# Optimization experiments

Measured on AMD Instinct MI355X. Metric: run time of the kernel, lower is better.

## Reference

```python
import jax, jax.numpy as jnp
import numpy as np

FACTOR = 0.1   # init_kwargs factor
EPS = 1e-7
B, C, H, W = 256, 3, 224, 224


def setup_inputs() -> dict:
    key = jax.random.key(0)
    k1, k2, k3 = jax.random.split(key, 3)
    x = jax.random.normal(k1, (B, C, H, W), dtype=jnp.float32)
    shift_fy = jax.random.uniform(k2, (B,), dtype=jnp.float32)  # maps to torch.rand(1)
    shift_fx = jax.random.uniform(k3, (B,), dtype=jnp.float32)
    return {"x": x, "shift_fy": shift_fy, "shift_fx": shift_fx}


def _shift_axis(img, shift, axis, size):
    # Equivalent to torch in-place slice copy + zero-fill:
    #   shift>0: img[..., :size-shift] = img[..., shift:]; img[..., size-shift:] = 0
    #   shift<0: img[..., -shift:]   = img[..., :shift];  img[..., :-shift]   = 0
    # == roll by -shift, then zero positions j where j+shift is out of [0, size)
    idx = jnp.arange(size)
    rolled = jnp.roll(img, -shift, axis=axis)
    mask = (idx + shift >= 0) & (idx + shift < size)
    shp = [1, 1, 1]
    shp[axis] = size
    return rolled * mask.reshape(shp).astype(img.dtype)


def _per_image(img, fy, fx):
    # img: [C, H, W]
    h, w = img.shape[1], img.shape[2]
    # int(shift_factor * size) truncates toward zero -> jnp.trunc
    sy = jnp.trunc((fy * 2.0 - 1.0) * FACTOR * h).astype(jnp.int32)
    sx = jnp.trunc((fx * 2.0 - 1.0) * FACTOR * w).astype(jnp.int32)
    img = _shift_axis(img, sy, 1, h)
    img = _shift_axis(img, sx, 2, w)
    # standardize with unbiased std (torch.std default, ddof=1)
    n = img.size
    mean = jnp.mean(img)
    var = jnp.sum(jnp.square(img - mean)) / (n - 1)
    img = (img - mean) / (jnp.sqrt(var) + EPS)
    # min-max normalize
    mn = jnp.min(img)
    mx = jnp.max(img)
    return (img - mn) / (mx - mn)


def reference(x, shift_fy, shift_fx):
    # fully vectorized over the batch (original uses a Python per-image loop)
    return jax.vmap(_per_image)(x, shift_fy, shift_fx)
```

## Files before the change

kernel.cpp:

```cpp
#include <hip/hip_runtime.h>
#include <math.h>


constexpr int kC = 3, kH = 224, kW = 224;
constexpr int kCHW = kC * kH * kW;
constexpr int kROWS = kC * kH;
constexpr int kQPR  = kW / 4;
constexpr int kNQ   = kROWS * kQPR;
constexpr int TB    = 256;
constexpr int PARTS = 8;

__device__ __forceinline__ void shifts_for(const float* __restrict__ sfy,
                                           const float* __restrict__ sfx,
                                           int img, int& sy, int& sx)
{
    float ty = sfy[img] * 2.0f - 1.0f; ty *= 0.1f; ty *= (float)kH;
    sy = (int)truncf(ty);
    float tx = sfx[img] * 2.0f - 1.0f; tx *= 0.1f; tx *= (float)kW;
    sx = (int)truncf(tx);
}

__global__ __launch_bounds__(TB) void minmax_k(
    const float* __restrict__ x, const float* __restrict__ sfy,
    const float* __restrict__ sfx, float2* __restrict__ ws)
{
    const int img  = blockIdx.x / PARTS;
    const int part = blockIdx.x - img * PARTS;
    const float* __restrict__ xb = x + (size_t)img * kCHW;

    int sy, sx; shifts_for(sfy, sfx, img, sy, sx);

    const int rlo = sy > 0 ? sy : 0;
    const int rhi = kH + (sy < 0 ? sy : 0);
    const int clo = sx > 0 ? sx : 0;
    const int chi = kW + (sx < 0 ? sx : 0);

    float vmin = INFINITY, vmax = -INFINITY;

    for (int f = part * TB + threadIdx.x; f < kNQ; f += PARTS * TB) {
        const int rr = f / kQPR;
        const int q  = f - rr * kQPR;
        const int j  = rr % kH;
        const bool rok = (j >= rlo) & (j < rhi);
        const float4 v4 = *(const float4*)(xb + rr * kW + q * 4);
        const float* v = (const float*)&v4;
        #pragma unroll
        for (int k = 0; k < 4; ++k) {
            const int i = q * 4 + k;
            const float val = (rok & (i >= clo) & (i < chi)) ? v[k] : 0.0f;
            vmin = fminf(vmin, val);
            vmax = fmaxf(vmax, val);
        }
    }

    #pragma unroll
    for (int off = 32; off > 0; off >>= 1) {
        vmin = fminf(vmin, __shfl_down(vmin, off));
        vmax = fmaxf(vmax, __shfl_down(vmax, off));
    }
    __shared__ float smin[TB / 64], smax[TB / 64];
    const int wave = threadIdx.x >> 6, lane = threadIdx.x & 63;
    if (lane == 0) { smin[wave] = vmin; smax[wave] = vmax; }
    __syncthreads();
    if (threadIdx.x == 0) {
        float mn = smin[0], mx = smax[0];
        #pragma unroll
        for (int w2 = 1; w2 < TB / 64; ++w2) {
            mn = fminf(mn, smin[w2]);
            mx = fmaxf(mx, smax[w2]);
        }
        ws[img * PARTS + part] = make_float2(mn, mx);
    }
}

template <int R>
__device__ __forceinline__ void gather_norm(const float* __restrict__ xb,
                                            float* __restrict__ ob,
                                            int sy, int sx, float mn, float inv,
                                            int f0)
{
    for (int f = f0; f < kNQ; f += PARTS * TB) {
        const int rr = f / kQPR;
        const int q  = f - rr * kQPR;
        const int j  = rr % kH;
        const int c0 = rr - j;
        const int jj = j + sy;
        const bool rowok = (unsigned)jj < (unsigned)kH;
        const int jc = rowok ? jj : 0;
        const float* __restrict__ src = xb + (c0 + jc) * kW;

        const int i0 = q * 4;
        const int base = i0 + sx - R;
        int qa = base;       qa = qa < 0 ? 0 : qa; qa = qa > kW - 4 ? kW - 4 : qa;
        int qb = base + 4;   qb = qb < 0 ? 0 : qb; qb = qb > kW - 4 ? kW - 4 : qb;
        const float4 av = *(const float4*)(src + qa);
        const float4 bv = *(const float4*)(src + qb);
        const float* a = (const float*)&av;
        const float* b = (const float*)&bv;

        float sel[4];
        #pragma unroll
        for (int k = 0; k < 4; ++k)
            sel[k] = (k + R < 4) ? a[k + R] : b[k + R - 4];

        float4 o;
        float* po = (float*)&o;
        #pragma unroll
        for (int k = 0; k < 4; ++k) {
            const int s = i0 + k + sx;
            const float v = (rowok && (unsigned)s < (unsigned)kW) ? sel[k] : 0.0f;
            po[k] = (v - mn) * inv;
        }
        *(float4*)(ob + rr * kW + i0) = o;
    }
}

__global__ __launch_bounds__(TB) void norm_k(
    const float* __restrict__ x, const float* __restrict__ sfy,
    const float* __restrict__ sfx, const float2* __restrict__ ws,
    float* __restrict__ out)
{
    const int img  = blockIdx.x / PARTS;
    const int part = blockIdx.x - img * PARTS;
    const float* __restrict__ xb = x + (size_t)img * kCHW;
    float* __restrict__ ob = out + (size_t)img * kCHW;

    int sy, sx; shifts_for(sfy, sfx, img, sy, sx);

    float mn = INFINITY, mx = -INFINITY;
    #pragma unroll
    for (int p = 0; p < PARTS; ++p) {
        const float2 v = ws[img * PARTS + p];
        mn = fminf(mn, v.x);
        mx = fmaxf(mx, v.y);
    }
    const float inv = 1.0f / (mx - mn);

    const int f0 = part * TB + threadIdx.x;
    switch (sx & 3) {
        case 0: gather_norm<0>(xb, ob, sy, sx, mn, inv, f0); break;
        case 1: gather_norm<1>(xb, ob, sy, sx, mn, inv, f0); break;
        case 2: gather_norm<2>(xb, ob, sy, sx, mn, inv, f0); break;
        default: gather_norm<3>(xb, ob, sy, sx, mn, inv, f0); break;
    }
}

extern "C" void kernel_launch(void* const* d_in, const int* in_sizes, int n_in,
                              void* d_out, int out_size, void* d_ws, size_t ws_size,
                              hipStream_t stream) {
    const float* x  = (const float*)d_in[0];
    const float* fy = (const float*)d_in[1];
    const float* fx = (const float*)d_in[2];
    float* out = (float*)d_out;
    const int B = in_sizes[1];
    float2* ws = (float2*)d_ws;
    minmax_k<<<B * PARTS, TB, 0, stream>>>(x, fy, fx, ws);
    norm_k<<<B * PARTS, TB, 0, stream>>>(x, fy, fx, ws, out);
}
```

Baseline: 301.5 us.

## Fuse min-max and normalize passes into one cooperative kernel with grid sync

Merges the two kernels into a single cooperative launch. Each block computes partial min/max, writes it to a device global, waits on a grid-wide sync, then does the shifted gather and normalization. PARTS drops to 4 so all 1024 blocks can be co-resident. Also unrolls the min-max load loop by 4 and switches to nontemporal stores. This removes a kernel launch and may keep part of the image in cache between passes, at the cost of a grid barrier and a residency requirement for the cooperative launch.

Result: slower. 421.6 us (+39.8%).

```diff
diff --git a/kernel.cpp b/kernel.cpp
--- a/kernel.cpp
+++ b/kernel.cpp
@@ -1,5 +1,8 @@
 #include <hip/hip_runtime.h>
+#include <hip/hip_cooperative_groups.h>
 #include <math.h>
+
+namespace cg = cooperative_groups;
 
 
 constexpr int kC = 3, kH = 224, kW = 224;
@@ -8,7 +11,12 @@
 constexpr int kQPR  = kW / 4;
 constexpr int kNQ   = kROWS * kQPR;
 constexpr int TB    = 256;
-constexpr int PARTS = 8;
+constexpr int PARTS = 4;
+constexpr int MAXB  = 256;
+
+typedef float f32x4 __attribute__((ext_vector_type(4)));
+
+__device__ float2 g_part[MAXB * PARTS];
 
 __device__ __forceinline__ void shifts_for(const float* __restrict__ sfy,
                                            const float* __restrict__ sfx,
@@ -20,65 +28,13 @@
     sx = (int)truncf(tx);
 }
 
-__global__ __launch_bounds__(TB) void minmax_k(
-    const float* __restrict__ x, const float* __restrict__ sfy,
-    const float* __restrict__ sfx, float2* __restrict__ ws)
-{
-    const int img  = blockIdx.x / PARTS;
-    const int part = blockIdx.x - img * PARTS;
-    const float* __restrict__ xb = x + (size_t)img * kCHW;
-
-    int sy, sx; shifts_for(sfy, sfx, img, sy, sx);
-
-    const int rlo = sy > 0 ? sy : 0;
-    const int rhi = kH + (sy < 0 ? sy : 0);
-    const int clo = sx > 0 ? sx : 0;
-    const int chi = kW + (sx < 0 ? sx : 0);
-
-    float vmin = INFINITY, vmax = -INFINITY;
-
-    for (int f = part * TB + threadIdx.x; f < kNQ; f += PARTS * TB) {
-        const int rr = f / kQPR;
-        const int q  = f - rr * kQPR;
-        const int j  = rr % kH;
-        const bool rok = (j >= rlo) & (j < rhi);
-        const float4 v4 = *(const float4*)(xb + rr * kW + q * 4);
-        const float* v = (const float*)&v4;
-        #pragma unroll
-        for (int k = 0; k < 4; ++k) {
-            const int i = q * 4 + k;
-            const float val = (rok & (i >= clo) & (i < chi)) ? v[k] : 0.0f;
-            vmin = fminf(vmin, val);
-            vmax = fmaxf(vmax, val);
-        }
-    }
-
-    #pragma unroll
-    for (int off = 32; off > 0; off >>= 1) {
-        vmin = fminf(vmin, __shfl_down(vmin, off));
-        vmax = fmaxf(vmax, __shfl_down(vmax, off));
-    }
-    __shared__ float smin[TB / 64], smax[TB / 64];
-    const int wave = threadIdx.x >> 6, lane = threadIdx.x & 63;
-    if (lane == 0) { smin[wave] = vmin; smax[wave] = vmax; }
-    __syncthreads();
-    if (threadIdx.x == 0) {
-        float mn = smin[0], mx = smax[0];
-        #pragma unroll
-        for (int w2 = 1; w2 < TB / 64; ++w2) {
-            mn = fminf(mn, smin[w2]);
-            mx = fmaxf(mx, smax[w2]);
-        }
-        ws[img * PARTS + part] = make_float2(mn, mx);
-    }
-}
-
 template <int R>
 __device__ __forceinline__ void gather_norm(const float* __restrict__ xb,
                                             float* __restrict__ ob,
                                             int sy, int sx, float mn, float inv,
                                             int f0)
 {
+    #pragma unroll 2
     for (int f = f0; f < kNQ; f += PARTS * TB) {
         const int rr = f / kQPR;
         const int q  = f - rr * kQPR;
@@ -103,45 +59,119 @@
         for (int k = 0; k < 4; ++k)
             sel[k] = (k + R < 4) ? a[k + R] : b[k + R - 4];
 
-        float4 o;
-        float* po = (float*)&o;
+        f32x4 o;
         #pragma unroll
         for (int k = 0; k < 4; ++k) {
             const int s = i0 + k + sx;
             const float v = (rowok && (unsigned)s < (unsigned)kW) ? sel[k] : 0.0f;
-            po[k] = (v - mn) * inv;
+            o[k] = (v - mn) * inv;
         }
-        *(float4*)(ob + rr * kW + i0) = o;
+        __builtin_nontemporal_store(o, (f32x4*)(ob + rr * kW + i0));
     }
 }
 
-__global__ __launch_bounds__(TB) void norm_k(
+__global__ __launch_bounds__(TB, 4) void shift_norm_coop(
     const float* __restrict__ x, const float* __restrict__ sfy,
-    const float* __restrict__ sfx, const float2* __restrict__ ws,
-    float* __restrict__ out)
+    const float* __restrict__ sfx, float* __restrict__ out)
 {
     const int img  = blockIdx.x / PARTS;
     const int part = blockIdx.x - img * PARTS;
     const float* __restrict__ xb = x + (size_t)img * kCHW;
     float* __restrict__ ob = out + (size_t)img * kCHW;
+    const int tid = threadIdx.x;
 
     int sy, sx; shifts_for(sfy, sfx, img, sy, sx);
 
-    float mn = INFINITY, mx = -INFINITY;
+    const int rlo = sy > 0 ? sy : 0;
+    const int rhi = kH + (sy < 0 ? sy : 0);
+    const int clo = sx > 0 ? sx : 0;
+    const int chi = kW + (sx < 0 ? sx : 0);
+
+    float vmin = INFINITY, vmax = -INFINITY;
+
+    constexpr int STR = PARTS * TB;
+    int f = part * TB + tid;
+    for (; f + 3 * STR < kNQ; f += 4 * STR) {
+        float4 v[4];
+        int  i0u[4];
+        bool roku[4];
+        #pragma unroll
+        for (int u = 0; u < 4; ++u) {
+            const int ff = f + u * STR;
+            const int rr = ff / kQPR;
+            const int q  = ff - rr * kQPR;
+            const int j  = rr % kH;
+            roku[u] = (j >= rlo) & (j < rhi);
+            i0u[u]  = q * 4;
+            v[u] = *(const float4*)(xb + rr * kW + q * 4);
+        }
+        #pragma unroll
+        for (int u = 0; u < 4; ++u) {
+            const float* vv = (const float*)&v[u];
+            #pragma unroll
+            for (int k = 0; k < 4; ++k) {
+                const int i = i0u[u] + k;
+                const float val = (roku[u] & (i >= clo) & (i < chi)) ? vv[k] : 0.0f;
+                vmin = fminf(vmin, val);
+                vmax = fmaxf(vmax, val);
+            }
+        }
+    }
+    for (; f < kNQ; f += STR) {
+        const int rr = f / kQPR;
+        const int q  = f - rr * kQPR;
+        const int j  = rr % kH;
+        const bool rok = (j >= rlo) & (j < rhi);
+        const float4 v4 = *(const float4*)(xb + rr * kW + q * 4);
+        const float* vv = (const float*)&v4;
+        #pragma unroll
+        for (int k = 0; k < 4; ++k) {
+            const int i = q * 4 + k;
+            const float val = (rok & (i >= clo) & (i < chi)) ? vv[k] : 0.0f;
+            vmin = fminf(vmin, val);
+            vmax = fmaxf(vmax, val);
+        }
+    }
+
     #pragma unroll
-    for (int p = 0; p < PARTS; ++p) {
-        const float2 v = ws[img * PARTS + p];
-        mn = fminf(mn, v.x);
-        mx = fmaxf(mx, v.y);
+    for (int off = 32; off > 0; off >>= 1) {
+        vmin = fminf(vmin, __shfl_down(vmin, off));
+        vmax = fmaxf(vmax, __shfl_down(vmax, off));
     }
-    const float inv = 1.0f / (mx - mn);
+    __shared__ float smin[TB / 64], smax[TB / 64];
+    const int wave = tid >> 6, lane = tid & 63;
+    if (lane == 0) { smin[wave] = vmin; smax[wave] = vmax; }
+    __syncthreads();
+    if (tid == 0) {
+        float mn = smin[0], mx = smax[0];
+        #pragma unroll
+        for (int w2 = 1; w2 < TB / 64; ++w2) {
+            mn = fminf(mn, smin[w2]);
+            mx = fmaxf(mx, smax[w2]);
+        }
+        g_part[blockIdx.x] = make_float2(mn, mx);
+    }
 
-    const int f0 = part * TB + threadIdx.x;
-    switch (sx & 3) {
-        case 0: gather_norm<0>(xb, ob, sy, sx, mn, inv, f0); break;
-        case 1: gather_norm<1>(xb, ob, sy, sx, mn, inv, f0); break;
-        case 2: gather_norm<2>(xb, ob, sy, sx, mn, inv, f0); break;
-        default: gather_norm<3>(xb, ob, sy, sx, mn, inv, f0); break;
+    cg::this_grid().sync();
+
+    {
+        const int p = tid & (PARTS - 1);
+        const float2 pv = g_part[img * PARTS + p];
+        float mn = pv.x, mx = pv.y;
+        #pragma unroll
+        for (int off = 1; off < PARTS; off <<= 1) {
+            mn = fminf(mn, __shfl_xor(mn, off));
+            mx = fmaxf(mx, __shfl_xor(mx, off));
+        }
+        const float inv = 1.0f / (mx - mn);
+
+        const int f0 = part * TB + tid;
+        switch (sx & 3) {
+            case 0: gather_norm<0>(xb, ob, sy, sx, mn, inv, f0); break;
+            case 1: gather_norm<1>(xb, ob, sy, sx, mn, inv, f0); break;
+            case 2: gather_norm<2>(xb, ob, sy, sx, mn, inv, f0); break;
+            default: gather_norm<3>(xb, ob, sy, sx, mn, inv, f0); break;
+        }
     }
 }
 
@@ -153,7 +183,7 @@
     const float* fx = (const float*)d_in[2];
     float* out = (float*)d_out;
     const int B = in_sizes[1];
-    float2* ws = (float2*)d_ws;
-    minmax_k<<<B * PARTS, TB, 0, stream>>>(x, fy, fx, ws);
-    norm_k<<<B * PARTS, TB, 0, stream>>>(x, fy, fx, ws, out);
+    void* args[] = { (void*)&x, (void*)&fy, (void*)&fx, (void*)&out };
+    hipLaunchCooperativeKernel((const void*)shift_norm_coop,
+                               dim3(B * PARTS), dim3(TB), args, 0, stream);
 }
```

## Map one wave per image row to drop index division and hoist column masks

Applied to the files above, without the earlier changes.

Both kernels now give each wavefront whole rows, with lanes 0-55 covering the 56 float4 quads of a row. The old flat-index loop with per-element divide and modulo is gone. Column masks, gather offsets and clamps are computed once per thread, and the normalize step becomes a single fma with a precomputed offset. In exchange, 8 of the 64 lanes in every wave sit idle (12.5% lane waste), and the uneven row distribution may reduce memory-level parallelism.

Result: faster. 295.3 us (-2.1%).

```diff
diff --git a/kernel.cpp b/kernel.cpp
--- a/kernel.cpp
+++ b/kernel.cpp
@@ -3,12 +3,16 @@
 
 
 constexpr int kC = 3, kH = 224, kW = 224;
-constexpr int kCHW = kC * kH * kW;
+constexpr int kCHW  = kC * kH * kW;
 constexpr int kROWS = kC * kH;
 constexpr int kQPR  = kW / 4;
-constexpr int kNQ   = kROWS * kQPR;
 constexpr int TB    = 256;
 constexpr int PARTS = 8;
+constexpr int WVB   = TB / 64;
+constexpr int WPI   = PARTS * WVB;
+constexpr int RPW   = kROWS / WPI;
+
+typedef float f32x4 __attribute__((ext_vector_type(4)));
 
 __device__ __forceinline__ void shifts_for(const float* __restrict__ sfy,
                                            const float* __restrict__ sfx,
@@ -35,21 +39,31 @@
     const int clo = sx > 0 ? sx : 0;
     const int chi = kW + (sx < 0 ? sx : 0);
 
+    const int tid  = threadIdx.x;
+    const int lane = tid & 63;
+    const int wv = __builtin_amdgcn_readfirstlane(tid >> 6) + part * WVB;
+
     float vmin = INFINITY, vmax = -INFINITY;
 
-    for (int f = part * TB + threadIdx.x; f < kNQ; f += PARTS * TB) {
-        const int rr = f / kQPR;
-        const int q  = f - rr * kQPR;
-        const int j  = rr % kH;
-        const bool rok = (j >= rlo) & (j < rhi);
-        const float4 v4 = *(const float4*)(xb + rr * kW + q * 4);
-        const float* v = (const float*)&v4;
+    if (lane < kQPR) {
+        const int i0 = lane * 4;
+        float cm[4];
         #pragma unroll
-        for (int k = 0; k < 4; ++k) {
-            const int i = q * 4 + k;
-            const float val = (rok & (i >= clo) & (i < chi)) ? v[k] : 0.0f;
-            vmin = fminf(vmin, val);
-            vmax = fmaxf(vmax, val);
+        for (int k = 0; k < 4; ++k)
+            cm[k] = ((i0 + k) >= clo && (i0 + k) < chi) ? 1.0f : 0.0f;
+
+        #pragma unroll 3
+        for (int t = 0; t < RPW; ++t) {
+            const int rr = wv + t * WPI;
+            const int j  = rr % kH;
+            const float srm = (j >= rlo && j < rhi) ? 1.0f : 0.0f;
+            const f32x4 v = *(const f32x4*)(xb + rr * kW + i0);
+            #pragma unroll
+            for (int k = 0; k < 4; ++k) {
+                const float val = v[k] * cm[k] * srm;
+                vmin = fminf(vmin, val);
+                vmax = fmaxf(vmax, val);
+            }
         }
     }
 
@@ -58,60 +72,62 @@
         vmin = fminf(vmin, __shfl_down(vmin, off));
         vmax = fmaxf(vmax, __shfl_down(vmax, off));
     }
-    __shared__ float smin[TB / 64], smax[TB / 64];
-    const int wave = threadIdx.x >> 6, lane = threadIdx.x & 63;
-    if (lane == 0) { smin[wave] = vmin; smax[wave] = vmax; }
+    __shared__ float smin[WVB], smax[WVB];
+    if (lane == 0) { smin[tid >> 6] = vmin; smax[tid >> 6] = vmax; }
     __syncthreads();
-    if (threadIdx.x == 0) {
+    if (tid == 0) {
         float mn = smin[0], mx = smax[0];
         #pragma unroll
-        for (int w2 = 1; w2 < TB / 64; ++w2) {
-            mn = fminf(mn, smin[w2]);
-            mx = fmaxf(mx, smax[w2]);
+        for (int w = 1; w < WVB; ++w) {
+            mn = fminf(mn, smin[w]);
+            mx = fmaxf(mx, smax[w]);
         }
         ws[img * PARTS + part] = make_float2(mn, mx);
     }
 }
 
 template <int R>
-__device__ __forceinline__ void gather_norm(const float* __restrict__ xb,
+__device__ __forceinline__ void gather_rows(const float* __restrict__ xb,
                                             float* __restrict__ ob,
-                                            int sy, int sx, float mn, float inv,
-                                            int f0)
+                                            int sy, int sx, float inv,
+                                            float zoff, int wv, int lane)
 {
-    for (int f = f0; f < kNQ; f += PARTS * TB) {
-        const int rr = f / kQPR;
-        const int q  = f - rr * kQPR;
+    if (lane >= kQPR) return;
+    const int i0   = lane * 4;
+    const int base = i0 + sx - R;
+    int qa = base;     qa = qa < 0 ? 0 : qa; qa = qa > kW - 4 ? kW - 4 : qa;
+    int qb = base + 4; qb = qb < 0 ? 0 : qb; qb = qb > kW - 4 ? kW - 4 : qb;
+
+    float cm[4];
+    #pragma unroll
+    for (int k = 0; k < 4; ++k) {
+        const int s = i0 + k + sx;
+        cm[k] = ((unsigned)s < (unsigned)kW) ? 1.0f : 0.0f;
+    }
+
+    #pragma unroll 3
+    for (int t = 0; t < RPW; ++t) {
+        const int rr = wv + t * WPI;
         const int j  = rr % kH;
         const int c0 = rr - j;
         const int jj = j + sy;
         const bool rowok = (unsigned)jj < (unsigned)kH;
         const int jc = rowok ? jj : 0;
+        const float scale = rowok ? inv : 0.0f;
         const float* __restrict__ src = xb + (c0 + jc) * kW;
 
-        const int i0 = q * 4;
-        const int base = i0 + sx - R;
-        int qa = base;       qa = qa < 0 ? 0 : qa; qa = qa > kW - 4 ? kW - 4 : qa;
-        int qb = base + 4;   qb = qb < 0 ? 0 : qb; qb = qb > kW - 4 ? kW - 4 : qb;
-        const float4 av = *(const float4*)(src + qa);
-        const float4 bv = *(const float4*)(src + qb);
-        const float* a = (const float*)&av;
-        const float* b = (const float*)&bv;
-
+        const f32x4 av = *(const f32x4*)(src + qa);
+        const f32x4 bv = *(const f32x4*)(src + qb);
         float sel[4];
         #pragma unroll
         for (int k = 0; k < 4; ++k)
-            sel[k] = (k + R < 4) ? a[k + R] : b[k + R - 4];
+            sel[k] = (k + R < 4) ? av[k + R] : bv[k + R - 4];
 
-        float4 o;
-        float* po = (float*)&o;
+        f32x4 o;
         #pragma unroll
-        for (int k = 0; k < 4; ++k) {
-            const int s = i0 + k + sx;
-            const float v = (rowok && (unsigned)s < (unsigned)kW) ? sel[k] : 0.0f;
-            po[k] = (v - mn) * inv;
-        }
-        *(float4*)(ob + rr * kW + i0) = o;
+        for (int k = 0; k < 4; ++k)
+            o[k] = fmaf(sel[k] * cm[k], scale, zoff);
+        *(f32x4*)(ob + rr * kW + i0) = o;
     }
 }
 
@@ -134,14 +150,17 @@
         mn = fminf(mn, v.x);
         mx = fmaxf(mx, v.y);
     }
-    const float inv = 1.0f / (mx - mn);
+    const float inv  = 1.0f / (mx - mn);
+    const float zoff = (0.0f - mn) * inv;
 
-    const int f0 = part * TB + threadIdx.x;
+    const int lane = threadIdx.x & 63;
+    const int wv = __builtin_amdgcn_readfirstlane(threadIdx.x >> 6) + part * WVB;
+
     switch (sx & 3) {
-        case 0: gather_norm<0>(xb, ob, sy, sx, mn, inv, f0); break;
-        case 1: gather_norm<1>(xb, ob, sy, sx, mn, inv, f0); break;
-        case 2: gather_norm<2>(xb, ob, sy, sx, mn, inv, f0); break;
-        default: gather_norm<3>(xb, ob, sy, sx, mn, inv, f0); break;
+        case 0: gather_rows<0>(xb, ob, sy, sx, inv, zoff, wv, lane); break;
+        case 1: gather_rows<1>(xb, ob, sy, sx, inv, zoff, wv, lane); break;
+        case 2: gather_rows<2>(xb, ob, sy, sx, inv, zoff, wv, lane); break;
+        default: gather_rows<3>(xb, ob, sy, sx, inv, zoff, wv, lane); break;
     }
 }
 
```
